# Kernel tuning notes

Measured on AMD Instinct MI355X. Metric: run time of the kernel, lower is better.

Reference implementation:

```python
import jax, jax.numpy as jnp
import numpy as np

L = 5          # num_layers
N = 50000      # nodes
E = 600000     # edges
D = 128        # num_features == hidden_units
G = 256        # graphs in batch
O = 10         # num_outputs
BN_EPS = 1e-5


def setup_inputs() -> dict:
    key = jax.random.key(0)
    ks = jax.random.split(key, 8)
    x = jax.random.normal(ks[0], (N, D), jnp.float32)
    edge_index = jax.random.randint(ks[1], (2, E), 0, N, jnp.int32)
    edge_attr = jax.random.randint(ks[2], (E, 3), 0, 8, jnp.int32)
    batch = jnp.sort(jax.random.randint(ks[3], (N,), 0, G, jnp.int32))
    s = 0.05
    return {
        "x": x,
        "edge_index": edge_index,
        "edge_attr": edge_attr,
        "batch": batch,
        "bond_emb": jax.random.normal(ks[4], (L, 3, 8, D), jnp.float32) * s,
        "conv_w1": jax.random.normal(ks[5], (L, D, D), jnp.float32) * s,
        "conv_b1": jnp.zeros((L, D), jnp.float32),
        "conv_bn_gamma": jnp.ones((L, D), jnp.float32),
        "conv_bn_beta": jnp.zeros((L, D), jnp.float32),
        "conv_bn_mean": jnp.zeros((L, D), jnp.float32),
        "conv_bn_var": jnp.ones((L, D), jnp.float32),
        "conv_w2": jax.random.normal(ks[6], (L, D, D), jnp.float32) * s,
        "conv_b2": jnp.zeros((L, D), jnp.float32),
        "bn_gamma": jnp.ones((L, D), jnp.float32),
        "bn_beta": jnp.zeros((L, D), jnp.float32),
        "bn_mean": jnp.zeros((L, D), jnp.float32),
        "bn_var": jnp.ones((L, D), jnp.float32),
        "fc_w": jax.random.normal(ks[7], (L + 1, D, O), jnp.float32) * s,
        "fc_b": jnp.zeros((L + 1, O), jnp.float32),
    }


def _bn_eval(h, gamma, beta, mean, var):
    return (h - mean) * jax.lax.rsqrt(var + BN_EPS) * gamma + beta


def reference(x, edge_index, edge_attr, batch, bond_emb,
              conv_w1, conv_b1, conv_bn_gamma, conv_bn_beta, conv_bn_mean, conv_bn_var,
              conv_w2, conv_b2, bn_gamma, bn_beta, bn_mean, bn_var, fc_w, fc_b):
    src, dst = edge_index[0], edge_index[1]  # x_j = x[src], aggregate at dst
    feat_ids = jnp.arange(3)
    outs = [x]
    for i in range(L):
        # BondEncoder: sum of per-feature embeddings -> [E, D]
        ea = bond_emb[i][feat_ids, edge_attr].sum(axis=1)
        # GINEConv (eps=0): msg = relu(x_j + edge_attr), scatter-add, nn(x + aggr)
        msg = jax.nn.relu(x[src] + ea)
        aggr = jax.ops.segment_sum(msg, dst, num_segments=N)
        h = x + aggr
        h = h @ conv_w1[i] + conv_b1[i]
        h = jax.nn.relu(_bn_eval(h, conv_bn_gamma[i], conv_bn_beta[i], conv_bn_mean[i], conv_bn_var[i]))
        h = h @ conv_w2[i] + conv_b2[i]
        x = jax.nn.relu(_bn_eval(h, bn_gamma[i], bn_beta[i], bn_mean[i], bn_var[i]))
        outs.append(x)
    # global mean pool per layer output, linear head, sum (dropout = identity in eval)
    counts = jax.ops.segment_sum(jnp.ones((N,), x.dtype), batch, num_segments=G)
    inv = 1.0 / jnp.maximum(counts, 1.0)
    out = jnp.zeros((G, O), x.dtype)
    for i, h in enumerate(outs):
        pooled = jax.ops.segment_sum(h, batch, num_segments=G) * inv[:, None]
        out = out + pooled @ fc_w[i] + fc_b[i]
    return out
```

## Files before the change

kernel.cpp:

```cpp
#include <hip/hip_runtime.h>

#define NN 50000
#define EE 600000
#define DD 128
#define GG 256
#define LL 5
#define OO 10
#define BN_EPS 1e-5f
#define CPAD 513
#define ESTRIDE 40
#define SENT (512u << 16)

#define B_SCAT  2344
#define B_COMBO 1283
#define B_WT    160
#define B_INV   1
#define B_CVTP  3125
#define B_PREP  (B_SCAT + B_COMBO + B_WT + B_INV + B_CVTP)

typedef __attribute__((ext_vector_type(8))) short short8;
typedef __attribute__((ext_vector_type(16))) float float16;

__device__ __forceinline__ unsigned short f2b(float f) {
    unsigned u = __float_as_uint(f);
    unsigned r = u + 0x7FFFu + ((u >> 16) & 1u);
    return (unsigned short)(r >> 16);
}
__device__ __forceinline__ unsigned pk2(float lo, float hi) {
    return (unsigned)f2b(lo) | ((unsigned)f2b(hi) << 16);
}
__device__ __forceinline__ float blo(unsigned u) { return __uint_as_float(u << 16); }
__device__ __forceinline__ float bhi(unsigned u) { return __uint_as_float(u & 0xFFFF0000u); }

__device__ __forceinline__ void acc8(float* acc, uint4 xv, uint4 cv) {
    acc[0] += fmaxf(blo(xv.x) + blo(cv.x), 0.f);
    acc[1] += fmaxf(bhi(xv.x) + bhi(cv.x), 0.f);
    acc[2] += fmaxf(blo(xv.y) + blo(cv.y), 0.f);
    acc[3] += fmaxf(bhi(xv.y) + bhi(cv.y), 0.f);
    acc[4] += fmaxf(blo(xv.z) + blo(cv.z), 0.f);
    acc[5] += fmaxf(bhi(xv.z) + bhi(cv.z), 0.f);
    acc[6] += fmaxf(blo(xv.w) + blo(cv.w), 0.f);
    acc[7] += fmaxf(bhi(xv.w) + bhi(cv.w), 0.f);
}

__launch_bounds__(256)
__global__ void prep(const float* __restrict__ x, const int* __restrict__ ei,
                     const int* __restrict__ eattr, const int* __restrict__ batch,
                     const float* __restrict__ bond,
                     const float* __restrict__ w1, const float* __restrict__ w2,
                     unsigned* __restrict__ xb4, unsigned short* __restrict__ combo,
                     short* __restrict__ wt, int* __restrict__ epos,
                     unsigned* __restrict__ e_info,
                     float* __restrict__ inv, float* __restrict__ pooled0) {
    const int bid = blockIdx.x, t = threadIdx.x;
    if (bid < B_SCAT) {
        int e = bid * 256 + t;
        if (e < EE) {
            int dst = ei[EE + e];
            int slot = atomicAdd(&epos[dst], 1);
            if (slot < ESTRIDE) {
                unsigned cidx = (unsigned)eattr[e * 3 + 0] | ((unsigned)eattr[e * 3 + 1] << 3)
                              | ((unsigned)eattr[e * 3 + 2] << 6);
                e_info[dst * ESTRIDE + slot] = (unsigned)ei[e] | (cidx << 16);
            }
        }
    } else if (bid < B_SCAT + B_COMBO) {
        int e = (bid - B_SCAT) * 256 + t;
        if (e < LL * CPAD * DD) {
            int l = e / (CPAD * DD), rem = e - l * (CPAD * DD);
            int c = rem / DD, d = rem - c * DD;
            float s;
            if (c == 512) s = -1e30f;
            else {
                const float* b_ = bond + (size_t)l * 3 * 8 * DD;
                s = b_[(c & 7) * DD + d] + b_[(8 + ((c >> 3) & 7)) * DD + d]
                  + b_[(16 + (c >> 6)) * DD + d];
            }
            combo[e] = f2b(s);
        }
    } else if (bid < B_SCAT + B_COMBO + B_WT) {
        __shared__ float tile[32][33];
        int b = bid - B_SCAT - B_COMBO;
        int mat = b >> 4, tl = b & 15;
        int k0 = (tl >> 2) * 32, c0 = (tl & 3) * 32;
        const float* W = (mat < 5) ? (w1 + (size_t)mat * DD * DD)
                                   : (w2 + (size_t)(mat - 5) * DD * DD);
        int j = t & 31, q = t >> 5;
#pragma unroll
        for (int rr = 0; rr < 4; ++rr) {
            int row = q + rr * 8;
            tile[row][j] = W[(size_t)(k0 + row) * DD + c0 + j];
        }
        __syncthreads();
#pragma unroll
        for (int rr = 0; rr < 4; ++rr) {
            int cr = q + rr * 8;
            wt[(size_t)mat * DD * DD + (size_t)(c0 + cr) * DD + k0 + j] = (short)f2b(tile[j][cr]);
        }
    } else if (bid < B_SCAT + B_COMBO + B_WT + B_INV) {
        __shared__ int sg[GG + 1];
        int g = t, lo = 0, hi = NN;
        while (lo < hi) { int m = (lo + hi) >> 1; if (batch[m] < g) lo = m + 1; else hi = m; }
        sg[g] = lo;
        if (g == 0) sg[GG] = NN;
        __syncthreads();
        inv[g] = 1.0f / fmaxf((float)(sg[g + 1] - sg[g]), 1.0f);
    } else {
        __shared__ float part[4][DD];
        int b = bid - (B_SCAT + B_COMBO + B_WT + B_INV);
        int gid = b * 256 + t;
        const float4* xp = (const float4*)(x + (size_t)gid * 8);
        float4 a = xp[0], c4 = xp[1];
        uint4 o;
        o.x = pk2(a.x, a.y); o.y = pk2(a.z, a.w);
        o.z = pk2(c4.x, c4.y); o.w = pk2(c4.z, c4.w);
        ((uint4*)xb4)[gid] = o;

        int row0 = b * 16;
        int row  = row0 + (t >> 4);
        int col8 = (t & 15) * 8;
        int gmin = batch[row0];
        int dg   = batch[row] - gmin;
        ((float*)part)[t] = 0.f;
        ((float*)part)[t + 256] = 0.f;
        __syncthreads();
        float v[8] = {a.x, a.y, a.z, a.w, c4.x, c4.y, c4.z, c4.w};
        if (dg < 4) {
#pragma unroll
            for (int j = 0; j < 8; ++j) atomicAdd(&part[dg][col8 + j], v[j]);
        } else {
#pragma unroll
            for (int j = 0; j < 8; ++j) atomicAdd(&pooled0[(gmin + dg) * DD + col8 + j], v[j]);
        }
        __syncthreads();
        for (int q2 = t; q2 < 4 * DD; q2 += 256) {
            int jj = q2 >> 7, c2 = q2 & 127;
            float pv = part[jj][c2];
            if (pv != 0.f && gmin + jj < GG) atomicAdd(&pooled0[(gmin + jj) * DD + c2], pv);
        }
    }
}

__launch_bounds__(256)
__global__ void aggr_csr(const unsigned short* __restrict__ xin,
                         const int* __restrict__ epos,
                         const unsigned* __restrict__ e_info,
                         const unsigned short* __restrict__ combo,
                         unsigned short* __restrict__ hin) {
    int node = blockIdx.x * 4 + (threadIdx.x >> 6);
    int lane = threadIdx.x & 63;
    if (node >= NN) return;
    const int base = node * ESTRIDE;
    int deg = epos[node]; if (deg > ESTRIDE) deg = ESTRIDE;
    const int eg = lane >> 4;
    const int f  = (lane & 15) * 8;

    unsigned i0 = e_info[base + eg];
    unsigned i1 = e_info[base + 4 + eg];
    unsigned i2 = e_info[base + 8 + eg];
    unsigned i3 = e_info[base + 12 + eg];
    if (eg      >= deg) i0 = SENT;
    if (4 + eg  >= deg) i1 = SENT;
    if (8 + eg  >= deg) i2 = SENT;
    if (12 + eg >= deg) i3 = SENT;

    uint4 xv0 = *(const uint4*)&xin[(size_t)(i0 & 0xFFFFu) * DD + f];
    uint4 cv0 = *(const uint4*)&combo[(size_t)(i0 >> 16) * DD + f];
    uint4 xv1 = *(const uint4*)&xin[(size_t)(i1 & 0xFFFFu) * DD + f];
    uint4 cv1 = *(const uint4*)&combo[(size_t)(i1 >> 16) * DD + f];
    uint4 xv2 = *(const uint4*)&xin[(size_t)(i2 & 0xFFFFu) * DD + f];
    uint4 cv2 = *(const uint4*)&combo[(size_t)(i2 >> 16) * DD + f];
    uint4 xv3 = *(const uint4*)&xin[(size_t)(i3 & 0xFFFFu) * DD + f];
    uint4 cv3 = *(const uint4*)&combo[(size_t)(i3 >> 16) * DD + f];

    float acc[8];
#pragma unroll
    for (int i = 0; i < 8; ++i) acc[i] = 0.f;
    acc8(acc, xv0, cv0);
    acc8(acc, xv1, cv1);
    acc8(acc, xv2, cv2);
    acc8(acc, xv3, cv3);

    if (deg > 16) {
        const int dend = base + deg;
        const int pe   = base + ((deg + 7) & ~7);
        for (int p = base + 16; p < pe; p += 8) {
            unsigned j0 = e_info[p + eg];
            unsigned j1 = e_info[p + 4 + eg];
            if (p + eg >= dend)     j0 = SENT;
            if (p + 4 + eg >= dend) j1 = SENT;
            uint4 ax0 = *(const uint4*)&xin[(size_t)(j0 & 0xFFFFu) * DD + f];
            uint4 ac0 = *(const uint4*)&combo[(size_t)(j0 >> 16) * DD + f];
            uint4 ax1 = *(const uint4*)&xin[(size_t)(j1 & 0xFFFFu) * DD + f];
            uint4 ac1 = *(const uint4*)&combo[(size_t)(j1 >> 16) * DD + f];
            acc8(acc, ax0, ac0);
            acc8(acc, ax1, ac1);
        }
    }

#pragma unroll
    for (int i = 0; i < 8; ++i) {
        acc[i] += __shfl_xor(acc[i], 16, 64);
        acc[i] += __shfl_xor(acc[i], 32, 64);
    }
    if (lane < 16) {
        uint4 self = *(const uint4*)&xin[(size_t)node * DD + f];
        uint4 o;
        o.x = pk2(acc[0] + blo(self.x), acc[1] + bhi(self.x));
        o.y = pk2(acc[2] + blo(self.y), acc[3] + bhi(self.y));
        o.z = pk2(acc[4] + blo(self.z), acc[5] + bhi(self.z));
        o.w = pk2(acc[6] + blo(self.w), acc[7] + bhi(self.w));
        *(uint4*)&hin[(size_t)node * DD + f] = o;
    }
}

__launch_bounds__(256)
__global__ void conv_fused(const unsigned short* __restrict__ hin,
                           const short* __restrict__ Wt1, const short* __restrict__ Wt2,
                           const float* __restrict__ b1, const float* __restrict__ g1,
                           const float* __restrict__ be1, const float* __restrict__ m1,
                           const float* __restrict__ v1,
                           const float* __restrict__ b2, const float* __restrict__ g2,
                           const float* __restrict__ be2, const float* __restrict__ m2,
                           const float* __restrict__ v2,
                           const int* __restrict__ batch,
                           unsigned short* __restrict__ outb,
                           float* __restrict__ pool_slot) {
    __shared__ short As[64 * 136];
    __shared__ int sbg[64];
    const int tid  = threadIdx.x;
    const int lane = tid & 63;
    const int wave = tid >> 6;
    const int row0 = blockIdx.x * 64;

    const int col   = wave * 32 + (lane & 31);
    const int khalf = (lane >> 5) * 8;
    const int arow  = lane & 31;
    const int rbase = 4 * (lane >> 5);
    const int gmin  = batch[row0];

    short8 bf[8];
#pragma unroll
    for (int ch = 0; ch < 8; ++ch)
        bf[ch] = *(const short8*)&Wt1[col * DD + ch * 16 + khalf];

    const float sc1 = g1[col] * rsqrtf(v1[col] + BN_EPS);
    const float sh1 = fmaf(b1[col] - m1[col], sc1, be1[col]);
    const float sc2 = g2[col] * rsqrtf(v2[col] + BN_EPS);
    const float sh2 = fmaf(b2[col] - m2[col], sc2, be2[col]);

    if (tid < 64) {
        int row = row0 + tid;
        sbg[tid] = (row < NN) ? batch[row] - gmin : -1;
    }
    for (int i = tid; i < 1024; i += 256) {
        int r = i >> 4, c8 = (i & 15) * 8;
        int row = row0 + r;
        uint4 z = make_uint4(0, 0, 0, 0);
        if (row < NN) z = *(const uint4*)&hin[(size_t)row * DD + c8];
        *(uint4*)&As[r * 136 + c8] = z;
    }
    __syncthreads();

    float16 acc0 = {0.f,0.f,0.f,0.f,0.f,0.f,0.f,0.f,0.f,0.f,0.f,0.f,0.f,0.f,0.f,0.f};
    float16 acc1 = acc0;
#pragma unroll
    for (int ch = 0; ch < 8; ++ch) {
        short8 a0 = *(const short8*)&As[(arow     ) * 136 + ch * 16 + khalf];
        short8 a1 = *(const short8*)&As[(32 + arow) * 136 + ch * 16 + khalf];
        acc0 = __builtin_amdgcn_mfma_f32_32x32x16_bf16(a0, bf[ch], acc0, 0, 0, 0);
        acc1 = __builtin_amdgcn_mfma_f32_32x32x16_bf16(a1, bf[ch], acc1, 0, 0, 0);
    }

#pragma unroll
    for (int ch = 0; ch < 8; ++ch)
        bf[ch] = *(const short8*)&Wt2[col * DD + ch * 16 + khalf];

    __syncthreads();
#pragma unroll
    for (int r = 0; r < 16; ++r) {
        int rl = (r & 3) + 8 * (r >> 2) + rbase;
        As[rl * 136 + col]        = (short)f2b(fmaxf(fmaf(acc0[r], sc1, sh1), 0.f));
        As[(32 + rl) * 136 + col] = (short)f2b(fmaxf(fmaf(acc1[r], sc1, sh1), 0.f));
    }
    __syncthreads();

    acc0 = acc1 = float16{0.f,0.f,0.f,0.f,0.f,0.f,0.f,0.f,0.f,0.f,0.f,0.f,0.f,0.f,0.f,0.f};
#pragma unroll
    for (int ch = 0; ch < 8; ++ch) {
        short8 a0 = *(const short8*)&As[(arow     ) * 136 + ch * 16 + khalf];
        short8 a1 = *(const short8*)&As[(32 + arow) * 136 + ch * 16 + khalf];
        acc0 = __builtin_amdgcn_mfma_f32_32x32x16_bf16(a0, bf[ch], acc0, 0, 0, 0);
        acc1 = __builtin_amdgcn_mfma_f32_32x32x16_bf16(a1, bf[ch], acc1, 0, 0, 0);
    }

    float pg0 = 0.f, pg1 = 0.f, pg2 = 0.f, pg3 = 0.f;
#pragma unroll
    for (int r = 0; r < 16; ++r) {
        int rl  = (r & 3) + 8 * (r >> 2) + rbase;
        int row = row0 + rl;
        float v0 = fmaxf(fmaf(acc0[r], sc2, sh2), 0.f);
        float v1_ = fmaxf(fmaf(acc1[r], sc2, sh2), 0.f);
        if (row < NN)      outb[(size_t)row * DD + col]        = f2b(v0);
        if (row + 32 < NN) outb[(size_t)(row + 32) * DD + col] = f2b(v1_);
        int ga = sbg[rl], gb = sbg[rl + 32];
        pg0 += ((ga == 0) ? v0 : 0.f) + ((gb == 0) ? v1_ : 0.f);
        pg1 += ((ga == 1) ? v0 : 0.f) + ((gb == 1) ? v1_ : 0.f);
        pg2 += ((ga == 2) ? v0 : 0.f) + ((gb == 2) ? v1_ : 0.f);
        pg3 += ((ga == 3) ? v0 : 0.f) + ((gb == 3) ? v1_ : 0.f);
    }
    pg0 += __shfl_down(pg0, 32);
    pg1 += __shfl_down(pg1, 32);
    pg2 += __shfl_down(pg2, 32);
    pg3 += __shfl_down(pg3, 32);
    if (lane < 32) {
        if (pg0 != 0.f)                  atomicAdd(&pool_slot[(gmin    ) * DD + col], pg0);
        if (pg1 != 0.f && gmin + 1 < GG) atomicAdd(&pool_slot[(gmin + 1) * DD + col], pg1);
        if (pg2 != 0.f && gmin + 2 < GG) atomicAdd(&pool_slot[(gmin + 2) * DD + col], pg2);
        if (pg3 != 0.f && gmin + 3 < GG) atomicAdd(&pool_slot[(gmin + 3) * DD + col], pg3);
    }
}

__launch_bounds__(64)
__global__ void head(const float* __restrict__ pooled, const float* __restrict__ inv,
                     const float* __restrict__ fcw, const float* __restrict__ fcb,
                     float* __restrict__ out) {
    int g = blockIdx.x, t = threadIdx.x;
    __shared__ float part[LL + 1][OO];
    if (t < (LL + 1) * OO) {
        int l = t / OO, o2 = t - l * OO;
        const float* p = pooled + ((size_t)l * GG + g) * DD;
        const float* w = fcw + (size_t)l * DD * OO + o2;
        float s = 0.f;
        for (int d2 = 0; d2 < DD; ++d2) s = fmaf(p[d2], w[(size_t)d2 * OO], s);
        part[l][o2] = s;
    }
    __syncthreads();
    if (t < OO) {
        float sp = 0.f, sb2 = 0.f;
#pragma unroll
        for (int l = 0; l < LL + 1; ++l) { sp += part[l][t]; sb2 += fcb[l * OO + t]; }
        out[g * OO + t] = sp * inv[g] + sb2;
    }
}

extern "C" void kernel_launch(void* const* d_in, const int* in_sizes, int n_in,
                              void* d_out, int out_size, void* d_ws, size_t ws_size,
                              hipStream_t stream) {
    const float* x_in    = (const float*)d_in[0];
    const int*   ei      = (const int*)d_in[1];
    const int*   eattr   = (const int*)d_in[2];
    const int*   batch   = (const int*)d_in[3];
    const float* bond    = (const float*)d_in[4];
    const float* conv_w1 = (const float*)d_in[5];
    const float* conv_b1 = (const float*)d_in[6];
    const float* cbg     = (const float*)d_in[7];
    const float* cbb     = (const float*)d_in[8];
    const float* cbm     = (const float*)d_in[9];
    const float* cbv     = (const float*)d_in[10];
    const float* conv_w2 = (const float*)d_in[11];
    const float* conv_b2 = (const float*)d_in[12];
    const float* bg      = (const float*)d_in[13];
    const float* bb      = (const float*)d_in[14];
    const float* bm      = (const float*)d_in[15];
    const float* bv      = (const float*)d_in[16];
    const float* fcw     = (const float*)d_in[17];
    const float* fcb     = (const float*)d_in[18];
    float* out = (float*)d_out;

    char* base = (char*)d_ws;
    size_t o = 0;
    auto carve = [&](size_t bytes) { void* p = base + o; o += (bytes + 15) & ~(size_t)15; return p; };
    unsigned short* xbA    = (unsigned short*)carve((size_t)NN * DD * 2);
    unsigned short* xbB    = (unsigned short*)carve((size_t)NN * DD * 2);
    unsigned short* combo  = (unsigned short*)carve((size_t)LL * CPAD * DD * 2);
    short*          wt     = (short*)carve((size_t)10 * DD * DD * 2);
    float*          inv    = (float*)carve(GG * 4);
    const size_t ZBYTES = (size_t)NN * 4 + (size_t)(LL + 1) * GG * DD * 4;
    int*            epos   = (int*)carve(ZBYTES);
    float*          pooled = (float*)((char*)epos + (size_t)NN * 4);
    unsigned*       e_info = (unsigned*)carve((size_t)NN * ESTRIDE * 4);

    hipMemsetAsync(epos, 0, ZBYTES, stream);

    prep<<<B_PREP, 256, 0, stream>>>(x_in, ei, eattr, batch, bond, conv_w1, conv_w2,
                                     (unsigned*)xbA, combo, wt, epos, e_info, inv, pooled);

    const int conv_blocks = (NN + 63) / 64;
    const int aggr_blocks = (NN + 3) / 4;
    unsigned short* xin  = xbA;
    unsigned short* xout = xbB;
    for (int i = 0; i < LL; ++i) {
        aggr_csr<<<aggr_blocks, 256, 0, stream>>>(
            xin, epos, e_info, combo + (size_t)i * CPAD * DD, xout);
        conv_fused<<<conv_blocks, 256, 0, stream>>>(
            xout, wt + (size_t)i * DD * DD, wt + (size_t)(5 + i) * DD * DD,
            conv_b1 + (size_t)i * DD, cbg + (size_t)i * DD, cbb + (size_t)i * DD,
            cbm + (size_t)i * DD, cbv + (size_t)i * DD,
            conv_b2 + (size_t)i * DD, bg + (size_t)i * DD, bb + (size_t)i * DD,
            bm + (size_t)i * DD, bv + (size_t)i * DD,
            batch, xin, pooled + (size_t)(i + 1) * GG * DD);
    }
    head<<<GG, 64, 0, stream>>>(pooled, inv, fcw, fcb, out);
}
```

Before: 419.5 us.

## Stage bond-embedding combo table in LDS with persistent aggregation blocks

The aggregation kernel becomes persistent: 256 blocks of 1024 threads, each handling 196 nodes. Each block first copies that layer's bf16 combo embedding table (513x128, about 131 KB) into shared memory, then gathers edge embeddings from LDS instead of global memory. The prep kernel also permutes its block index order to spread the different work types across the grid. The large LDS footprint limits each CU to one block with 16 waves, and only 256 blocks are launched, so latency hiding for the random x gathers may drop.

Measured after the change: 434.4 us. +3.6%, slower.

```diff
diff --git a/kernel.cpp b/kernel.cpp
--- a/kernel.cpp
+++ b/kernel.cpp
@@ -18,6 +18,10 @@
 #define B_CVTP  3125
 #define B_PREP  (B_SCAT + B_COMBO + B_WT + B_INV + B_CVTP)
 
+#define AGGR_BLOCKS  256
+#define AGGR_THREADS 1024
+#define NPB 196
+
 typedef __attribute__((ext_vector_type(8))) short short8;
 typedef __attribute__((ext_vector_type(16))) float float16;
 
@@ -52,7 +56,8 @@
                      short* __restrict__ wt, int* __restrict__ epos,
                      unsigned* __restrict__ e_info,
                      float* __restrict__ inv, float* __restrict__ pooled0) {
-    const int bid = blockIdx.x, t = threadIdx.x;
+    const int bid = (int)(((long long)blockIdx.x * 1021) % B_PREP);
+    const int t = threadIdx.x;
     if (bid < B_SCAT) {
         int e = bid * 256 + t;
         if (e < EE) {
@@ -141,76 +146,91 @@
     }
 }
 
-__launch_bounds__(256)
+__launch_bounds__(AGGR_THREADS)
 __global__ void aggr_csr(const unsigned short* __restrict__ xin,
                          const int* __restrict__ epos,
                          const unsigned* __restrict__ e_info,
                          const unsigned short* __restrict__ combo,
                          unsigned short* __restrict__ hin) {
-    int node = blockIdx.x * 4 + (threadIdx.x >> 6);
-    int lane = threadIdx.x & 63;
-    if (node >= NN) return;
-    const int base = node * ESTRIDE;
-    int deg = epos[node]; if (deg > ESTRIDE) deg = ESTRIDE;
+    __shared__ unsigned short cl[CPAD * DD];
+    const int tid = threadIdx.x;
+    {
+        const uint4* cg = (const uint4*)combo;
+        uint4* cs = (uint4*)cl;
+        for (int i = tid; i < CPAD * DD / 8; i += AGGR_THREADS) cs[i] = cg[i];
+    }
+    __syncthreads();
+
+    const int wave = tid >> 6;
+    const int lane = tid & 63;
     const int eg = lane >> 4;
     const int f  = (lane & 15) * 8;
 
-    unsigned i0 = e_info[base + eg];
-    unsigned i1 = e_info[base + 4 + eg];
-    unsigned i2 = e_info[base + 8 + eg];
-    unsigned i3 = e_info[base + 12 + eg];
-    if (eg      >= deg) i0 = SENT;
-    if (4 + eg  >= deg) i1 = SENT;
-    if (8 + eg  >= deg) i2 = SENT;
-    if (12 + eg >= deg) i3 = SENT;
-
-    uint4 xv0 = *(const uint4*)&xin[(size_t)(i0 & 0xFFFFu) * DD + f];
-    uint4 cv0 = *(const uint4*)&combo[(size_t)(i0 >> 16) * DD + f];
-    uint4 xv1 = *(const uint4*)&xin[(size_t)(i1 & 0xFFFFu) * DD + f];
-    uint4 cv1 = *(const uint4*)&combo[(size_t)(i1 >> 16) * DD + f];
-    uint4 xv2 = *(const uint4*)&xin[(size_t)(i2 & 0xFFFFu) * DD + f];
-    uint4 cv2 = *(const uint4*)&combo[(size_t)(i2 >> 16) * DD + f];
-    uint4 xv3 = *(const uint4*)&xin[(size_t)(i3 & 0xFFFFu) * DD + f];
-    uint4 cv3 = *(const uint4*)&combo[(size_t)(i3 >> 16) * DD + f];
-
-    float acc[8];
-#pragma unroll
-    for (int i = 0; i < 8; ++i) acc[i] = 0.f;
-    acc8(acc, xv0, cv0);
-    acc8(acc, xv1, cv1);
-    acc8(acc, xv2, cv2);
-    acc8(acc, xv3, cv3);
-
-    if (deg > 16) {
-        const int dend = base + deg;
-        const int pe   = base + ((deg + 7) & ~7);
-        for (int p = base + 16; p < pe; p += 8) {
-            unsigned j0 = e_info[p + eg];
-            unsigned j1 = e_info[p + 4 + eg];
-            if (p + eg >= dend)     j0 = SENT;
-            if (p + 4 + eg >= dend) j1 = SENT;
-            uint4 ax0 = *(const uint4*)&xin[(size_t)(j0 & 0xFFFFu) * DD + f];
-            uint4 ac0 = *(const uint4*)&combo[(size_t)(j0 >> 16) * DD + f];
-            uint4 ax1 = *(const uint4*)&xin[(size_t)(j1 & 0xFFFFu) * DD + f];
-            uint4 ac1 = *(const uint4*)&combo[(size_t)(j1 >> 16) * DD + f];
-            acc8(acc, ax0, ac0);
-            acc8(acc, ax1, ac1);
-        }
-    }
-
-#pragma unroll
-    for (int i = 0; i < 8; ++i) {
-        acc[i] += __shfl_xor(acc[i], 16, 64);
-        acc[i] += __shfl_xor(acc[i], 32, 64);
-    }
-    if (lane < 16) {
-        uint4 self = *(const uint4*)&xin[(size_t)node * DD + f];
-        uint4 o;
-        o.x = pk2(acc[0] + blo(self.x), acc[1] + bhi(self.x));
-        o.y = pk2(acc[2] + blo(self.y), acc[3] + bhi(self.y));
-        o.z = pk2(acc[4] + blo(self.z), acc[5] + bhi(self.z));
-        o.w = pk2(acc[6] + blo(self.w), acc[7] + bhi(self.w));
-        *(uint4*)&hin[(size_t)node * DD + f] = o;
+    for (int it = 0; it < (NPB + 15) / 16; ++it) {
+        const int ln = it * 16 + wave;
+        const int node = blockIdx.x * NPB + ln;
+        if (ln >= NPB || node >= NN) continue;
+
+        const int base = node * ESTRIDE;
+        int deg = epos[node]; if (deg > ESTRIDE) deg = ESTRIDE;
+
+        unsigned i0 = e_info[base + eg];
+        unsigned i1 = e_info[base + 4 + eg];
+        unsigned i2 = e_info[base + 8 + eg];
+        unsigned i3 = e_info[base + 12 + eg];
+        if (eg      >= deg) i0 = SENT;
+        if (4 + eg  >= deg) i1 = SENT;
+        if (8 + eg  >= deg) i2 = SENT;
+        if (12 + eg >= deg) i3 = SENT;
+
+        uint4 xv0 = *(const uint4*)&xin[(size_t)(i0 & 0xFFFFu) * DD + f];
+        uint4 cv0 = *(const uint4*)&cl[(i0 >> 16) * DD + f];
+        uint4 xv1 = *(const uint4*)&xin[(size_t)(i1 & 0xFFFFu) * DD + f];
+        uint4 cv1 = *(const uint4*)&cl[(i1 >> 16) * DD + f];
+        uint4 xv2 = *(const uint4*)&xin[(size_t)(i2 & 0xFFFFu) * DD + f];
+        uint4 cv2 = *(const uint4*)&cl[(i2 >> 16) * DD + f];
+        uint4 xv3 = *(const uint4*)&xin[(size_t)(i3 & 0xFFFFu) * DD + f];
+        uint4 cv3 = *(const uint4*)&cl[(i3 >> 16) * DD + f];
+
+        float acc[8];
+#pragma unroll
+        for (int i = 0; i < 8; ++i) acc[i] = 0.f;
+        acc8(acc, xv0, cv0);
+        acc8(acc, xv1, cv1);
+        acc8(acc, xv2, cv2);
+        acc8(acc, xv3, cv3);
+
+        if (deg > 16) {
+            const int dend = base + deg;
+            const int pe   = base + ((deg + 7) & ~7);
+            for (int p = base + 16; p < pe; p += 8) {
+                unsigned j0 = e_info[p + eg];
+                unsigned j1 = e_info[p + 4 + eg];
+                if (p + eg >= dend)     j0 = SENT;
+                if (p + 4 + eg >= dend) j1 = SENT;
+                uint4 ax0 = *(const uint4*)&xin[(size_t)(j0 & 0xFFFFu) * DD + f];
+                uint4 ac0 = *(const uint4*)&cl[(j0 >> 16) * DD + f];
+                uint4 ax1 = *(const uint4*)&xin[(size_t)(j1 & 0xFFFFu) * DD + f];
+                uint4 ac1 = *(const uint4*)&cl[(j1 >> 16) * DD + f];
+                acc8(acc, ax0, ac0);
+                acc8(acc, ax1, ac1);
+            }
+        }
+
+#pragma unroll
+        for (int i = 0; i < 8; ++i) {
+            acc[i] += __shfl_xor(acc[i], 16, 64);
+            acc[i] += __shfl_xor(acc[i], 32, 64);
+        }
+        if (lane < 16) {
+            uint4 self = *(const uint4*)&xin[(size_t)node * DD + f];
+            uint4 o;
+            o.x = pk2(acc[0] + blo(self.x), acc[1] + bhi(self.x));
+            o.y = pk2(acc[2] + blo(self.y), acc[3] + bhi(self.y));
+            o.z = pk2(acc[4] + blo(self.z), acc[5] + bhi(self.z));
+            o.w = pk2(acc[6] + blo(self.w), acc[7] + bhi(self.w));
+            *(uint4*)&hin[(size_t)node * DD + f] = o;
+        }
     }
 }
 
@@ -387,11 +407,10 @@
                                      (unsigned*)xbA, combo, wt, epos, e_info, inv, pooled);
 
     const int conv_blocks = (NN + 63) / 64;
-    const int aggr_blocks = (NN + 3) / 4;
     unsigned short* xin  = xbA;
     unsigned short* xout = xbB;
     for (int i = 0; i < LL; ++i) {
-        aggr_csr<<<aggr_blocks, 256, 0, stream>>>(
+        aggr_csr<<<AGGR_BLOCKS, AGGR_THREADS, 0, stream>>>(
             xin, epos, e_info, combo + (size_t)i * CPAD * DD, xout);
         conv_fused<<<conv_blocks, 256, 0, stream>>>(
             xout, wt + (size_t)i * DD * DD, wt + (size_t)(5 + i) * DD * DD,
```
